# Optimization experiments

Measured on AMD Instinct MI355X. Metric: run time of the kernel, lower is better.

Reference implementation:

```python
import jax, jax.numpy as jnp
import numpy as np

B, LMAX, NCOND, NHID = 256, 512, 300, 600

def setup_inputs() -> dict:
    key = jax.random.key(0)
    ks = jax.random.split(key, 7)
    x = jax.random.normal(ks[0], (B, NCOND), dtype=jnp.float32)
    context = jax.random.normal(ks[1], (B, LMAX, NCOND), dtype=jnp.float32)
    lengths = jax.random.randint(ks[2], (B,), 0, LMAX, dtype=jnp.int32)
    W1 = jax.random.normal(ks[3], (NCOND, NHID), dtype=jnp.float32) * (1.0 / np.sqrt(NCOND))
    b1 = jax.random.normal(ks[4], (NHID,), dtype=jnp.float32) * 0.02
    Wa = jax.random.normal(ks[5], (NHID, NCOND), dtype=jnp.float32) * (1.0 / np.sqrt(NHID))
    ba = jax.random.normal(ks[6], (NCOND,), dtype=jnp.float32) * 0.02
    return {"x": x, "context": context, "lengths": lengths, "W1": W1, "b1": b1, "Wa": Wa, "ba": ba}

def reference(x, context, lengths, W1, b1, Wa, ba):
    # lengths clamped to >=1 (a ragged context is always non-empty)
    lens = jnp.maximum(lengths, 1)
    # valid-position mask over padded context: [B, L, 1]
    valid = (jnp.arange(LMAX)[None, :] < lens[:, None])[..., None].astype(context.dtype)
    # per-token MLP: relu(ctx @ W1 + b1)  -> [B, L, nhid]
    h = jax.nn.relu(jnp.einsum('blc,ch->blh', context, W1) + b1)
    # masked mean over valid tokens (ragged mean-pool) -> [B, nhid]
    pooled = jnp.sum(h * valid, axis=1) / lens[:, None].astype(context.dtype)
    # sigmoid gate -> [B, ncond], applied to x embeddings
    gate = jax.nn.sigmoid(jnp.einsum('bh,hc->bc', pooled, Wa) + ba)
    return gate * x
```

## Files before the change

kernel.cpp:

```cpp
#include <hip/hip_runtime.h>
#include <math.h>

#define BB     256
#define LMAX   512
#define NCOND  300
#define NHID   600
#define NSEG   8
#define CHUNK  64
#define KPAD   320
#define KLDS   328
#define NKC    10

typedef short s16x8 __attribute__((ext_vector_type(8)));
typedef float f32x4 __attribute__((ext_vector_type(4)));

__device__ inline unsigned short f2bf(float f) {
    unsigned int x = __float_as_uint(f);
    x += 0x7fffu + ((x >> 16) & 1u);
    return (unsigned short)(x >> 16);
}

__global__ __launch_bounds__(256) void k0_w1t(const float* __restrict__ W1,
                                              unsigned short* __restrict__ w1t)
{
    const int t     = blockIdx.x * 256 + threadIdx.x;
    const int lane  = t & 63;
    const int g     = t >> 6;
    const int ntile = g / NKC;
    const int kc    = g - ntile * NKC;
    const int n     = ntile * 16 + (lane & 15);
    const int kbase = kc * 32 + (lane >> 4) * 8;
    union { unsigned short us[8]; s16x8 v8; } u;
#pragma unroll
    for (int j = 0; j < 8; ++j) {
        const int k = kbase + j;
        const float w = (n < NHID && k < NCOND) ? W1[(size_t)k * NHID + n] : 0.f;
        u.us[j] = f2bf(w);
    }
    *(s16x8*)(w1t + (size_t)t * 8) = u.v8;
}

__global__ __launch_bounds__(512, 4) void k1_mfma_pool(
    const float* __restrict__ ctx, const int* __restrict__ lengths,
    const unsigned short* __restrict__ w1t, const float* __restrict__ b1,
    float* __restrict__ partial)
{
    const int b  = blockIdx.x;
    const int s  = blockIdx.y;
    const int ch = blockIdx.z;

    int count = lengths[b]; if (count < 1) count = 1;
    const int l0 = s * CHUNK;
    if (l0 >= count) return;
    const int valid = min(count - l0, CHUNK);

    const int tid  = threadIdx.x;
    const int lane = tid & 63;
    const int wv   = tid >> 6;
    const int ln15 = lane & 15;
    const int kg   = lane >> 4;

    __shared__ __align__(16) unsigned short atile[CHUNK * KLDS];

    {
        const int r      = tid >> 3;
        const int c8base = tid & 7;
        const bool inrow = (r < valid);
        const float* rowp = ctx + ((size_t)b * LMAX + l0 + r) * NCOND;
#pragma unroll
        for (int p = 0; p < 5; ++p) {
            const int c8 = c8base + p * 8;
            float4 v0 = make_float4(0.f, 0.f, 0.f, 0.f);
            float4 v1 = make_float4(0.f, 0.f, 0.f, 0.f);
            if (inrow && c8 <= 37) v0 = *(const float4*)(rowp + c8 * 8);
            if (inrow && c8 <= 36) v1 = *(const float4*)(rowp + c8 * 8 + 4);
            union { unsigned short us[8]; s16x8 v8; } u;
            u.us[0] = f2bf(v0.x); u.us[1] = f2bf(v0.y);
            u.us[2] = f2bf(v0.z); u.us[3] = f2bf(v0.w);
            u.us[4] = f2bf(v1.x); u.us[5] = f2bf(v1.y);
            u.us[6] = f2bf(v1.z); u.us[7] = f2bf(v1.w);
            *(s16x8*)(atile + r * KLDS + c8 * 8) = u.v8;
        }
    }
    __syncthreads();

    const int ntg   = wv >> 1;
    const int mrow0 = (wv & 1) * 32;
    const int ntile0 = ch * 20 + ntg * 5;
    const unsigned short* bbase = w1t + ((size_t)ntile0 * NKC * 64 + lane) * 8;
    const unsigned short* arow  = atile + (mrow0 + ln15) * KLDS + kg * 8;

    f32x4 acc[5][2];
#pragma unroll
    for (int nt = 0; nt < 5; ++nt)
#pragma unroll
        for (int mt = 0; mt < 2; ++mt) acc[nt][mt] = (f32x4){0.f, 0.f, 0.f, 0.f};

    s16x8 bf[2][5];
#pragma unroll
    for (int nt = 0; nt < 5; ++nt) bf[0][nt] = *(const s16x8*)(bbase + nt * 5120);

#pragma unroll
    for (int kc = 0; kc < NKC; ++kc) {
        const int cur = kc & 1, nxt = cur ^ 1;
        if (kc < NKC - 1) {
#pragma unroll
            for (int nt = 0; nt < 5; ++nt)
                bf[nxt][nt] = *(const s16x8*)(bbase + nt * 5120 + (kc + 1) * 512);
        }
        s16x8 af[2];
#pragma unroll
        for (int mt = 0; mt < 2; ++mt)
            af[mt] = *(const s16x8*)(arow + mt * 16 * KLDS + kc * 32);
#pragma unroll
        for (int nt = 0; nt < 5; ++nt)
#pragma unroll
            for (int mt = 0; mt < 2; ++mt)
                acc[nt][mt] = __builtin_amdgcn_mfma_f32_16x16x32_bf16(
                    af[mt], bf[cur][nt], acc[nt][mt], 0, 0, 0);
    }

    __syncthreads();
    float* psums = (float*)atile;

    float wsum[5];
#pragma unroll
    for (int nt = 0; nt < 5; ++nt) {
        const int colg = ch * 320 + ntg * 80 + nt * 16 + ln15;
        const float b1c = (colg < NHID) ? b1[colg] : 0.f;
        float ssum = 0.f;
#pragma unroll
        for (int mt = 0; mt < 2; ++mt) {
            const int rbase = mrow0 + mt * 16 + kg * 4;
#pragma unroll
            for (int r = 0; r < 4; ++r) {
                const float h = fmaxf(acc[nt][mt][r] + b1c, 0.f);
                if (rbase + r < valid) ssum += h;
            }
        }
        ssum += __shfl_xor(ssum, 16, 64);
        ssum += __shfl_xor(ssum, 32, 64);
        wsum[nt] = ssum;
    }
    if (kg == 0) {
#pragma unroll
        for (int nt = 0; nt < 5; ++nt)
            psums[(wv * 5 + nt) * 16 + ln15] = wsum[nt];
    }
    __syncthreads();

    if ((wv & 1) == 0 && kg == 0) {
#pragma unroll
        for (int nt = 0; nt < 5; ++nt) {
            const float tot = psums[(wv * 5 + nt) * 16 + ln15]
                            + psums[((wv + 1) * 5 + nt) * 16 + ln15];
            const int colg = ch * 320 + ntg * 80 + nt * 16 + ln15;
            if (colg < NHID)
                partial[((size_t)s * BB + b) * NHID + colg] = tot;
        }
    }
}

__global__ __launch_bounds__(640) void k2_gate(
    const float* __restrict__ x, const int* __restrict__ lengths,
    const float* __restrict__ partial, const float* __restrict__ Wa,
    const float* __restrict__ ba, float* __restrict__ out)
{
    const int b0  = blockIdx.x * 2;
    const int tid = threadIdx.x;

    __shared__ float pl[2][NHID];

    if (tid < NHID) {
#pragma unroll
        for (int bb = 0; bb < 2; ++bb) {
            int count = lengths[b0 + bb]; if (count < 1) count = 1;
            const int nch = (count + CHUNK - 1) >> 6;
            float ssum = 0.f;
            for (int sp = 0; sp < nch; ++sp)
                ssum += partial[((size_t)sp * BB + (b0 + bb)) * NHID + tid];
            pl[bb][tid] = ssum / (float)count;
        }
    }
    __syncthreads();

    if (tid < 2 * NCOND) {
        const int bb = tid / NCOND;
        const int n  = tid - bb * NCOND;
        const int b  = b0 + bb;
        float a0 = ba[n], a1 = 0.f, a2 = 0.f, a3 = 0.f;
        const float4* p4 = (const float4*)pl[bb];
        for (int h4 = 0; h4 < 148; h4 += 4) {
            const float4 pv0 = p4[h4];
            const float4 pv1 = p4[h4 + 1];
            const float4 pv2 = p4[h4 + 2];
            const float4 pv3 = p4[h4 + 3];
            const int hb = h4 * 4;
            a0 = fmaf(pv0.x, Wa[(size_t)(hb +  0) * NCOND + n], a0);
            a0 = fmaf(pv0.y, Wa[(size_t)(hb +  1) * NCOND + n], a0);
            a0 = fmaf(pv0.z, Wa[(size_t)(hb +  2) * NCOND + n], a0);
            a0 = fmaf(pv0.w, Wa[(size_t)(hb +  3) * NCOND + n], a0);
            a1 = fmaf(pv1.x, Wa[(size_t)(hb +  4) * NCOND + n], a1);
            a1 = fmaf(pv1.y, Wa[(size_t)(hb +  5) * NCOND + n], a1);
            a1 = fmaf(pv1.z, Wa[(size_t)(hb +  6) * NCOND + n], a1);
            a1 = fmaf(pv1.w, Wa[(size_t)(hb +  7) * NCOND + n], a1);
            a2 = fmaf(pv2.x, Wa[(size_t)(hb +  8) * NCOND + n], a2);
            a2 = fmaf(pv2.y, Wa[(size_t)(hb +  9) * NCOND + n], a2);
            a2 = fmaf(pv2.z, Wa[(size_t)(hb + 10) * NCOND + n], a2);
            a2 = fmaf(pv2.w, Wa[(size_t)(hb + 11) * NCOND + n], a2);
            a3 = fmaf(pv3.x, Wa[(size_t)(hb + 12) * NCOND + n], a3);
            a3 = fmaf(pv3.y, Wa[(size_t)(hb + 13) * NCOND + n], a3);
            a3 = fmaf(pv3.z, Wa[(size_t)(hb + 14) * NCOND + n], a3);
            a3 = fmaf(pv3.w, Wa[(size_t)(hb + 15) * NCOND + n], a3);
        }
        {
            const float4 pv0 = p4[148];
            const float4 pv1 = p4[149];
            a0 = fmaf(pv0.x, Wa[(size_t)592 * NCOND + n], a0);
            a0 = fmaf(pv0.y, Wa[(size_t)593 * NCOND + n], a0);
            a0 = fmaf(pv0.z, Wa[(size_t)594 * NCOND + n], a0);
            a0 = fmaf(pv0.w, Wa[(size_t)595 * NCOND + n], a0);
            a1 = fmaf(pv1.x, Wa[(size_t)596 * NCOND + n], a1);
            a1 = fmaf(pv1.y, Wa[(size_t)597 * NCOND + n], a1);
            a1 = fmaf(pv1.z, Wa[(size_t)598 * NCOND + n], a1);
            a1 = fmaf(pv1.w, Wa[(size_t)599 * NCOND + n], a1);
        }
        const float acc  = (a0 + a1) + (a2 + a3);
        const float gate = 1.0f / (1.0f + expf(-acc));
        out[(size_t)b * NCOND + n] = gate * x[(size_t)b * NCOND + n];
    }
}

extern "C" void kernel_launch(void* const* d_in, const int* in_sizes, int n_in,
                              void* d_out, int out_size, void* d_ws, size_t ws_size,
                              hipStream_t stream)
{
    const float* x       = (const float*)d_in[0];
    const float* ctx     = (const float*)d_in[1];
    const int*   lengths = (const int*)  d_in[2];
    const float* W1      = (const float*)d_in[3];
    const float* b1      = (const float*)d_in[4];
    const float* Wa      = (const float*)d_in[5];
    const float* ba      = (const float*)d_in[6];
    float*       out     = (float*)d_out;

    unsigned short* w1t     = (unsigned short*)d_ws;
    float*          partial = (float*)((char*)d_ws + 409600);

    k0_w1t<<<100, 256, 0, stream>>>(W1, w1t);
    k1_mfma_pool<<<dim3(BB, NSEG, 2), 512, 0, stream>>>(ctx, lengths, w1t, b1, partial);
    k2_gate<<<BB / 2, 640, 0, stream>>>(x, lengths, partial, Wa, ba, out);
}
```

Measured before the change: 307.0 us.

## Make pooling kernel persistent over strided chunks with register prefetch of next chunk

The MFMA pooling kernel now launches 4 blocks per (batch, half) of 256 threads instead of 8 segments of 512 threads. Each block loops over 32-row chunks strided by 4, accumulating the masked ReLU sums in registers. While the current chunk is in LDS and going through MFMA, the block prefetches the next chunk's context into registers, overlapping global loads with compute. This cuts block count, partial-sum writes and the cross-wave LDS reduction, but adds extra barriers per chunk and reloads the W1 fragments every chunk.

```diff
diff --git a/kernel.cpp b/kernel.cpp
--- a/kernel.cpp
+++ b/kernel.cpp
@@ -5,8 +5,8 @@
 #define LMAX   512
 #define NCOND  300
 #define NHID   600
-#define NSEG   8
-#define CHUNK  64
+#define CHUNK  32
+#define NPG    4
 #define KPAD   320
 #define KLDS   328
 #define NKC    10
@@ -40,19 +40,17 @@
     *(s16x8*)(w1t + (size_t)t * 8) = u.v8;
 }
 
-__global__ __launch_bounds__(512, 4) void k1_mfma_pool(
+__global__ __launch_bounds__(256, 3) void k1_mfma_pool(
     const float* __restrict__ ctx, const int* __restrict__ lengths,
     const unsigned short* __restrict__ w1t, const float* __restrict__ b1,
     float* __restrict__ partial)
 {
     const int b  = blockIdx.x;
-    const int s  = blockIdx.y;
+    const int p  = blockIdx.y;
     const int ch = blockIdx.z;
 
     int count = lengths[b]; if (count < 1) count = 1;
-    const int l0 = s * CHUNK;
-    if (l0 >= count) return;
-    const int valid = min(count - l0, CHUNK);
+    if (p * CHUNK >= count) return;
 
     const int tid  = threadIdx.x;
     const int lane = tid & 63;
@@ -62,18 +60,51 @@
 
     __shared__ __align__(16) unsigned short atile[CHUNK * KLDS];
 
+    const int r      = tid >> 3;
+    const int c8base = tid & 7;
+
+    const int ntile0 = ch * 20 + wv * 5;
+    const unsigned short* bbase = w1t + ((size_t)ntile0 * NKC * 64 + lane) * 8;
+    const unsigned short* arow  = atile + ln15 * KLDS + kg * 8;
+
+    float b1c[5];
+#pragma unroll
+    for (int nt = 0; nt < 5; ++nt) {
+        const int colg = ch * 320 + wv * 80 + nt * 16 + ln15;
+        b1c[nt] = (colg < NHID) ? b1[colg] : 0.f;
+    }
+
+    float psum[5] = {0.f, 0.f, 0.f, 0.f, 0.f};
+
+    int c = p;
+    float4 ld[10];
     {
-        const int r      = tid >> 3;
-        const int c8base = tid & 7;
+        const int l0 = c * CHUNK;
+        const int valid = min(count - l0, CHUNK);
         const bool inrow = (r < valid);
         const float* rowp = ctx + ((size_t)b * LMAX + l0 + r) * NCOND;
 #pragma unroll
-        for (int p = 0; p < 5; ++p) {
-            const int c8 = c8base + p * 8;
+        for (int q = 0; q < 5; ++q) {
+            const int c8 = c8base + q * 8;
             float4 v0 = make_float4(0.f, 0.f, 0.f, 0.f);
             float4 v1 = make_float4(0.f, 0.f, 0.f, 0.f);
             if (inrow && c8 <= 37) v0 = *(const float4*)(rowp + c8 * 8);
             if (inrow && c8 <= 36) v1 = *(const float4*)(rowp + c8 * 8 + 4);
+            ld[2 * q] = v0; ld[2 * q + 1] = v1;
+        }
+    }
+
+    for (;;) {
+        const int l0    = c * CHUNK;
+        const int valid = min(count - l0, CHUNK);
+
+        __syncthreads();
+
+#pragma unroll
+        for (int q = 0; q < 5; ++q) {
+            const int c8 = c8base + q * 8;
+            const float4 v0 = ld[2 * q];
+            const float4 v1 = ld[2 * q + 1];
             union { unsigned short us[8]; s16x8 v8; } u;
             u.us[0] = f2bf(v0.x); u.us[1] = f2bf(v0.y);
             u.us[2] = f2bf(v0.z); u.us[3] = f2bf(v0.w);
@@ -81,82 +112,85 @@
             u.us[6] = f2bf(v1.z); u.us[7] = f2bf(v1.w);
             *(s16x8*)(atile + r * KLDS + c8 * 8) = u.v8;
         }
-    }
-    __syncthreads();
-
-    const int ntg   = wv >> 1;
-    const int mrow0 = (wv & 1) * 32;
-    const int ntile0 = ch * 20 + ntg * 5;
-    const unsigned short* bbase = w1t + ((size_t)ntile0 * NKC * 64 + lane) * 8;
-    const unsigned short* arow  = atile + (mrow0 + ln15) * KLDS + kg * 8;
-
-    f32x4 acc[5][2];
-#pragma unroll
-    for (int nt = 0; nt < 5; ++nt)
-#pragma unroll
-        for (int mt = 0; mt < 2; ++mt) acc[nt][mt] = (f32x4){0.f, 0.f, 0.f, 0.f};
-
-    s16x8 bf[2][5];
-#pragma unroll
-    for (int nt = 0; nt < 5; ++nt) bf[0][nt] = *(const s16x8*)(bbase + nt * 5120);
-
-#pragma unroll
-    for (int kc = 0; kc < NKC; ++kc) {
-        const int cur = kc & 1, nxt = cur ^ 1;
-        if (kc < NKC - 1) {
+
+        const int cn = c + NPG;
+        const bool more = (cn * CHUNK < count);
+        if (more) {
+            const int l0n = cn * CHUNK;
+            const int vn  = min(count - l0n, CHUNK);
+            const bool inrow = (r < vn);
+            const float* rowp = ctx + ((size_t)b * LMAX + l0n + r) * NCOND;
+#pragma unroll
+            for (int q = 0; q < 5; ++q) {
+                const int c8 = c8base + q * 8;
+                float4 v0 = make_float4(0.f, 0.f, 0.f, 0.f);
+                float4 v1 = make_float4(0.f, 0.f, 0.f, 0.f);
+                if (inrow && c8 <= 37) v0 = *(const float4*)(rowp + c8 * 8);
+                if (inrow && c8 <= 36) v1 = *(const float4*)(rowp + c8 * 8 + 4);
+                ld[2 * q] = v0; ld[2 * q + 1] = v1;
+            }
+        }
+
+        __syncthreads();
+
+        f32x4 acc[5][2];
+#pragma unroll
+        for (int nt = 0; nt < 5; ++nt)
+#pragma unroll
+            for (int mt = 0; mt < 2; ++mt) acc[nt][mt] = (f32x4){0.f, 0.f, 0.f, 0.f};
+
+        s16x8 bf[2][5];
+#pragma unroll
+        for (int nt = 0; nt < 5; ++nt) bf[0][nt] = *(const s16x8*)(bbase + nt * 5120);
+
+#pragma unroll
+        for (int kc = 0; kc < NKC; ++kc) {
+            const int cur = kc & 1, nxt = cur ^ 1;
+            if (kc < NKC - 1) {
+#pragma unroll
+                for (int nt = 0; nt < 5; ++nt)
+                    bf[nxt][nt] = *(const s16x8*)(bbase + nt * 5120 + (kc + 1) * 512);
+            }
+            s16x8 af[2];
+#pragma unroll
+            for (int mt = 0; mt < 2; ++mt)
+                af[mt] = *(const s16x8*)(arow + mt * 16 * KLDS + kc * 32);
 #pragma unroll
             for (int nt = 0; nt < 5; ++nt)
-                bf[nxt][nt] = *(const s16x8*)(bbase + nt * 5120 + (kc + 1) * 512);
-        }
-        s16x8 af[2];
-#pragma unroll
-        for (int mt = 0; mt < 2; ++mt)
-            af[mt] = *(const s16x8*)(arow + mt * 16 * KLDS + kc * 32);
-#pragma unroll
-        for (int nt = 0; nt < 5; ++nt)
-#pragma unroll
-            for (int mt = 0; mt < 2; ++mt)
-                acc[nt][mt] = __builtin_amdgcn_mfma_f32_16x16x32_bf16(
-                    af[mt], bf[cur][nt], acc[nt][mt], 0, 0, 0);
-    }
-
-    __syncthreads();
-    float* psums = (float*)atile;
-
-    float wsum[5];
+#pragma unroll
+                for (int mt = 0; mt < 2; ++mt)
+                    acc[nt][mt] = __builtin_amdgcn_mfma_f32_16x16x32_bf16(
+                        af[mt], bf[cur][nt], acc[nt][mt], 0, 0, 0);
+        }
+
+#pragma unroll
+        for (int nt = 0; nt < 5; ++nt) {
+            float s = 0.f;
+#pragma unroll
+            for (int mt = 0; mt < 2; ++mt) {
+                const int rbase = mt * 16 + kg * 4;
+#pragma unroll
+                for (int rr = 0; rr < 4; ++rr) {
+                    const float h = fmaxf(acc[nt][mt][rr] + b1c[nt], 0.f);
+                    if (rbase + rr < valid) s += h;
+                }
+            }
+            psum[nt] += s;
+        }
+
+        if (!more) break;
+        c = cn;
+    }
+
 #pragma unroll
     for (int nt = 0; nt < 5; ++nt) {
-        const int colg = ch * 320 + ntg * 80 + nt * 16 + ln15;
-        const float b1c = (colg < NHID) ? b1[colg] : 0.f;
-        float ssum = 0.f;
-#pragma unroll
-        for (int mt = 0; mt < 2; ++mt) {
-            const int rbase = mrow0 + mt * 16 + kg * 4;
-#pragma unroll
-            for (int r = 0; r < 4; ++r) {
-                const float h = fmaxf(acc[nt][mt][r] + b1c, 0.f);
-                if (rbase + r < valid) ssum += h;
-            }
-        }
-        ssum += __shfl_xor(ssum, 16, 64);
-        ssum += __shfl_xor(ssum, 32, 64);
-        wsum[nt] = ssum;
-    }
-    if (kg == 0) {
-#pragma unroll
-        for (int nt = 0; nt < 5; ++nt)
-            psums[(wv * 5 + nt) * 16 + ln15] = wsum[nt];
-    }
-    __syncthreads();
-
-    if ((wv & 1) == 0 && kg == 0) {
-#pragma unroll
-        for (int nt = 0; nt < 5; ++nt) {
-            const float tot = psums[(wv * 5 + nt) * 16 + ln15]
-                            + psums[((wv + 1) * 5 + nt) * 16 + ln15];
-            const int colg = ch * 320 + ntg * 80 + nt * 16 + ln15;
+        float s = psum[nt];
+        s += __shfl_xor(s, 16, 64);
+        s += __shfl_xor(s, 32, 64);
+        if (kg == 0) {
+            const int colg = ch * 320 + wv * 80 + nt * 16 + ln15;
             if (colg < NHID)
-                partial[((size_t)s * BB + b) * NHID + colg] = tot;
+                partial[((size_t)p * BB + b) * NHID + colg] = s;
         }
     }
 }
@@ -175,9 +209,9 @@
 #pragma unroll
         for (int bb = 0; bb < 2; ++bb) {
             int count = lengths[b0 + bb]; if (count < 1) count = 1;
-            const int nch = (count + CHUNK - 1) >> 6;
+            const int nslots = min((count + CHUNK - 1) / CHUNK, NPG);
             float ssum = 0.f;
-            for (int sp = 0; sp < nch; ++sp)
+            for (int sp = 0; sp < nslots; ++sp)
                 ssum += partial[((size_t)sp * BB + (b0 + bb)) * NHID + tid];
             pl[bb][tid] = ssum / (float)count;
         }
@@ -248,6 +282,6 @@
     float*          partial = (float*)((char*)d_ws + 409600);
 
     k0_w1t<<<100, 256, 0, stream>>>(W1, w1t);
-    k1_mfma_pool<<<dim3(BB, NSEG, 2), 512, 0, stream>>>(ctx, lengths, w1t, b1, partial);
+    k1_mfma_pool<<<dim3(BB, NPG, 2), 256, 0, stream>>>(ctx, lengths, w1t, b1, partial);
     k2_gate<<<BB / 2, 640, 0, stream>>>(x, lengths, partial, Wa, ba, out);
 }
```

Result: slower. 482.1 us (+57.0%).
